# Kernel optimization log

Measured on AMD Instinct MI355X. Metric: run time of the kernel, lower is better.

Reference implementation:

```python
import jax, jax.numpy as jnp
import numpy as np

B, N, H = 8, 1024, 768
INNER = 64
ENT = 9
NEG = 1e12


def setup_inputs() -> dict:
    key = jax.random.key(0)
    ks = jax.random.split(key, 4)
    return {
        "last_hidden_state": jax.random.normal(ks[0], (B, N, H), dtype=jnp.float32),
        "attention_mask": jnp.ones((B, N), dtype=jnp.float32),
        "w1": jax.random.normal(ks[1], (H, 2 * INNER), dtype=jnp.float32) * 0.02,
        "b1": jnp.zeros((2 * INNER,), dtype=jnp.float32),
        "w2": jax.random.normal(ks[2], (H, 2 * ENT), dtype=jnp.float32) * 0.02,
        "b2": jnp.zeros((2 * ENT,), dtype=jnp.float32),
    }


def reference(last_hidden_state, attention_mask, w1, b1, w2, b2):
    b, n, _ = last_hidden_state.shape
    outputs = last_hidden_state @ w1 + b1            # (b, n, 2*inner)
    qw, kw = outputs[..., ::2], outputs[..., 1::2]   # (b, n, inner) each

    # Sinusoidal RoPE, 'zero' merge mode: even slots sin, odd slots cos
    half = INNER // 2
    inv_freq = jnp.power(10000.0, -2.0 * jnp.arange(half, dtype=jnp.float32) / INNER)
    ang = jnp.arange(n, dtype=jnp.float32)[:, None] * inv_freq[None, :]  # (n, half)
    sin_pos = jnp.repeat(jnp.sin(ang), 2, axis=-1)[None]  # (1, n, inner)
    cos_pos = jnp.repeat(jnp.cos(ang), 2, axis=-1)[None]

    def rope(x):
        # interleave (-x_odd, x_even)
        x2 = jnp.stack([-x[..., 1::2], x[..., ::2]], axis=-1).reshape(x.shape)
        return x * cos_pos + x2 * sin_pos

    qw, kw = rope(qw), rope(kw)

    logits = jnp.einsum('bmd,bnd->bmn', qw, kw) / jnp.sqrt(jnp.float32(INNER))
    bias = jnp.einsum('bnh->bhn', last_hidden_state @ w2 + b2) / 2.0  # (b, 2*ent, n)
    logits = logits[:, None] + bias[:, ::2, None] + bias[:, 1::2, :, None]  # (b,ent,n,n)

    # sequence masking on both trailing axes
    m = attention_mask.astype(logits.dtype)
    m_row = m[:, None, :, None]
    m_col = m[:, None, None, :]
    logits = logits * m_row + (-NEG) * (1.0 - m_row)
    logits = logits * m_col + (-NEG) * (1.0 - m_col)

    # strict lower-triangular suppression
    tril = jnp.tril(jnp.ones((n, n), dtype=logits.dtype), k=-1)
    logits = logits - tril * NEG
    return logits
```

## Files before the change

kernel.cpp:

```cpp
#include <hip/hip_runtime.h>
#include <cmath>

constexpr int kB = 8;
constexpr int kN = 1024;
constexpr int kH = 768;
constexpr float kNeg = 1000000000000.0f;

__global__ __launch_bounds__(256) void k1_proj_rope(
    const float* __restrict__ lhs, const float* __restrict__ w1,
    const float* __restrict__ b1, const float* __restrict__ w2,
    const float* __restrict__ b2, float* __restrict__ qw,
    float* __restrict__ kw, float* __restrict__ biasT)
{
  __shared__ float xs[16][kH];
  const int t = threadIdx.x;
  const int g0 = blockIdx.x * 16;

  const float4* lhs4 = reinterpret_cast<const float4*>(lhs + (size_t)g0 * kH);
  float4* xs4 = reinterpret_cast<float4*>(&xs[0][0]);
#pragma unroll
  for (int p = 0; p < 12; ++p) xs4[t + p * 256] = lhs4[t + p * 256];
  __syncthreads();

  const int c = t & 31;
  const int r2 = t >> 5;
  float acc0[4] = {0.f, 0.f, 0.f, 0.f};
  float acc1[4] = {0.f, 0.f, 0.f, 0.f};
  const float* xr0 = xs[r2];
  const float* xr1 = xs[r2 + 8];
  for (int h = 0; h < kH; h += 4) {
    float x0[4], x1[4];
    *reinterpret_cast<float4*>(x0) = *reinterpret_cast<const float4*>(&xr0[h]);
    *reinterpret_cast<float4*>(x1) = *reinterpret_cast<const float4*>(&xr1[h]);
#pragma unroll
    for (int hh = 0; hh < 4; ++hh) {
      const float4 wv =
          *reinterpret_cast<const float4*>(&w1[(size_t)(h + hh) * 128 + 4 * c]);
      acc0[0] += x0[hh] * wv.x; acc0[1] += x0[hh] * wv.y;
      acc0[2] += x0[hh] * wv.z; acc0[3] += x0[hh] * wv.w;
      acc1[0] += x1[hh] * wv.x; acc1[1] += x1[hh] * wv.y;
      acc1[2] += x1[hh] * wv.z; acc1[3] += x1[hh] * wv.w;
    }
  }
  float bb[4];
  *reinterpret_cast<float4*>(bb) = *reinterpret_cast<const float4*>(&b1[4 * c]);

  const float inv = exp2f(-(float)c * 0.41524101186092f);
#pragma unroll
  for (int rr = 0; rr < 2; ++rr) {
    const float* acc = rr ? acc1 : acc0;
    const int g = g0 + r2 + rr * 8;
    const int n = g & (kN - 1);
    float si, co;
    sincosf((float)n * inv, &si, &co);
    const float oq0 = acc[0] + bb[0], ok0 = acc[1] + bb[1];
    const float oq1 = acc[2] + bb[2], ok1 = acc[3] + bb[3];
    float2 qv = make_float2(oq0 * co - oq1 * si, oq1 * co + oq0 * si);
    float2 kv = make_float2(ok0 * co - ok1 * si, ok1 * co + ok0 * si);
    *reinterpret_cast<float2*>(&qw[(size_t)g * 64 + 2 * c]) = qv;
    *reinterpret_cast<float2*>(&kw[(size_t)g * 64 + 2 * c]) = kv;
  }

  for (int idx = t; idx < 288; idx += 256) {
    const int row = idx / 18, col = idx % 18;
    float s = 0.f;
    for (int h = 0; h < kH; h += 4) {
      const float4 xv = *reinterpret_cast<const float4*>(&xs[row][h]);
      s += xv.x * w2[(size_t)h * 18 + col];
      s += xv.y * w2[(size_t)(h + 1) * 18 + col];
      s += xv.z * w2[(size_t)(h + 2) * 18 + col];
      s += xv.w * w2[(size_t)(h + 3) * 18 + col];
    }
    const int g = g0 + row;
    const int b = g >> 10, n = g & (kN - 1);
    biasT[((size_t)b * 18 + col) * kN + n] = (s + b2[col]) * 0.5f;
  }
}

__global__ __launch_bounds__(256) void k2_logits(
    const float* __restrict__ qw, const float* __restrict__ kw,
    const float* __restrict__ biasT, const float* __restrict__ mask,
    float* __restrict__ out)
{
  constexpr int LD = 68;
  __shared__ float smem[64 * LD * 2 + 576 * 2 + 128];
  float* qs = smem;
  float* ks = smem + 64 * LD;
  float* ts = smem;
  float* bE = smem + 128 * LD;
  float* bO = bE + 576;
  float* mr_s = bO + 576;
  float* mc_s = mr_s + 64;

  const int t = threadIdx.x;
  const int b = blockIdx.z;
  const int m0 = blockIdx.y * 64;
  const int n0 = blockIdx.x * 64;

  const float* qg = qw + ((size_t)b * kN + m0) * 64;
  const float* kg = kw + ((size_t)b * kN + n0) * 64;
#pragma unroll
  for (int p = 0; p < 4; ++p) {
    const int idx = t + p * 256;
    const int row = idx >> 4;
    const int c4 = (idx & 15) << 2;
    *reinterpret_cast<float4*>(&qs[row * LD + c4]) =
        *reinterpret_cast<const float4*>(&qg[row * 64 + c4]);
    *reinterpret_cast<float4*>(&ks[row * LD + c4]) =
        *reinterpret_cast<const float4*>(&kg[row * 64 + c4]);
  }
  for (int idx = t; idx < 576; idx += 256) {
    const int e = idx >> 6, x = idx & 63;
    bE[idx] = biasT[((size_t)b * 18 + 2 * e) * kN + n0 + x];
    bO[idx] = biasT[((size_t)b * 18 + 2 * e + 1) * kN + m0 + x];
  }
  if (t < 64) mr_s[t] = mask[b * kN + m0 + t];
  else if (t < 128) mc_s[t - 64] = mask[b * kN + n0 + (t - 64)];
  __syncthreads();

  const int tx = t & 15;
  const int ty = t >> 4;
  const int ml = ty << 2;

  float acc[4][4] = {};
  for (int d = 0; d < 64; d += 4) {
    float4 q[4], k[4];
#pragma unroll
    for (int i = 0; i < 4; ++i)
      q[i] = *reinterpret_cast<const float4*>(&qs[(ml + i) * LD + d]);
#pragma unroll
    for (int j = 0; j < 4; ++j)
      k[j] = *reinterpret_cast<const float4*>(&ks[(tx + 16 * j) * LD + d]);
#pragma unroll
    for (int i = 0; i < 4; ++i)
#pragma unroll
      for (int j = 0; j < 4; ++j)
        acc[i][j] += q[i].x * k[j].x + q[i].y * k[j].y +
                     q[i].z * k[j].z + q[i].w * k[j].w;
  }

  __syncthreads();
#pragma unroll
  for (int i = 0; i < 4; ++i)
#pragma unroll
    for (int j = 0; j < 4; ++j)
      ts[(ml + i) * LD + tx + 16 * j] = acc[i][j] * 0.125f;
  __syncthreads();

  const int rb = ml;
  const int cb = tx << 2;
  float4 sv[4];
#pragma unroll
  for (int i = 0; i < 4; ++i)
    sv[i] = *reinterpret_cast<const float4*>(&ts[(rb + i) * LD + cb]);

  const float4 mrv = *reinterpret_cast<const float4*>(&mr_s[rb]);
  const float4 mcv = *reinterpret_cast<const float4*>(&mc_s[cb]);
  const float mrA[4] = {mrv.x, mrv.y, mrv.z, mrv.w};
  const float mcA[4] = {mcv.x, mcv.y, mcv.z, mcv.w};

  const size_t obase =
      (size_t)b * 9 * kN * kN + (size_t)(m0 + rb) * kN + (n0 + cb);
  for (int e = 0; e < 9; ++e) {
    const float4 bev = *reinterpret_cast<const float4*>(&bE[e * 64 + cb]);
    const float4 bov = *reinterpret_cast<const float4*>(&bO[e * 64 + rb]);
    const float beA[4] = {bev.x, bev.y, bev.z, bev.w};
    const float boA[4] = {bov.x, bov.y, bov.z, bov.w};
    float* oe = out + obase + (size_t)e * kN * kN;
#pragma unroll
    for (int i = 0; i < 4; ++i) {
      const int m = m0 + rb + i;
      const float* s = reinterpret_cast<const float*>(&sv[i]);
      float4 v4;
      float* v = reinterpret_cast<float*>(&v4);
#pragma unroll
      for (int c = 0; c < 4; ++c) {
        const int n = n0 + cb + c;
        float val = s[c] + beA[c] + boA[i];
        val = val * mrA[i] - kNeg * (1.f - mrA[i]);
        val = val * mcA[c] - kNeg * (1.f - mcA[c]);
        if (m > n) val -= kNeg;
        v[c] = val;
      }
      *reinterpret_cast<float4*>(&oe[(size_t)i * kN]) = v4;
    }
  }
}

extern "C" void kernel_launch(void* const* d_in, const int* in_sizes, int n_in,
                              void* d_out, int out_size, void* d_ws, size_t ws_size,
                              hipStream_t stream) {
  const float* lhs  = (const float*)d_in[0];
  const float* mask = (const float*)d_in[1];
  const float* w1   = (const float*)d_in[2];
  const float* b1   = (const float*)d_in[3];
  const float* w2   = (const float*)d_in[4];
  const float* b2   = (const float*)d_in[5];
  float* out = (float*)d_out;

  float* qw    = (float*)d_ws;
  float* kwp   = qw  + (size_t)kB * kN * 64;
  float* biasT = kwp + (size_t)kB * kN * 64;

  k1_proj_rope<<<dim3(kB * kN / 16), 256, 0, stream>>>(lhs, w1, b1, w2, b2,
                                                       qw, kwp, biasT);
  k2_logits<<<dim3(kN / 64, kN / 64, kB), 256, 0, stream>>>(qw, kwp, biasT,
                                                            mask, out);
}
```

Baseline: 428.9 us.

## Stage w1 chunks in shared memory and process 32 rows per projection block

The projection kernel now walks the hidden dimension in 96-wide chunks, staging each w1 chunk and the matching activation slice in shared memory, so w1 is read from LDS instead of global memory. Blocks grow to 512 threads covering 32 rows, and the w2 bias projection is spread over all threads chunk by chunk instead of being a serial tail done by a few threads. The output kernel only gets a loop variable renamed. The catch is an extra barrier per chunk and fewer blocks, while the dominant cost remains the large output write in the second kernel.

```diff
diff --git a/kernel.cpp b/kernel.cpp
--- a/kernel.cpp
+++ b/kernel.cpp
@@ -6,50 +6,93 @@
 constexpr int kH = 768;
 constexpr float kNeg = 1000000000000.0f;
 
-__global__ __launch_bounds__(256) void k1_proj_rope(
+__global__ __launch_bounds__(512) void k1_proj_rope(
     const float* __restrict__ lhs, const float* __restrict__ w1,
     const float* __restrict__ b1, const float* __restrict__ w2,
     const float* __restrict__ b2, float* __restrict__ qw,
     float* __restrict__ kw, float* __restrict__ biasT)
 {
-  __shared__ float xs[16][kH];
+  constexpr int CH = 96;
+  constexpr int XP = 100;
+  __shared__ float ws1[CH * 128];
+  __shared__ float xs[32 * XP];
+
   const int t = threadIdx.x;
-  const int g0 = blockIdx.x * 16;
-
-  const float4* lhs4 = reinterpret_cast<const float4*>(lhs + (size_t)g0 * kH);
-  float4* xs4 = reinterpret_cast<float4*>(&xs[0][0]);
-#pragma unroll
-  for (int p = 0; p < 12; ++p) xs4[t + p * 256] = lhs4[t + p * 256];
-  __syncthreads();
-
+  const int g0 = blockIdx.x * 32;
   const int c = t & 31;
-  const int r2 = t >> 5;
+  const int rp = t >> 5;
+
   float acc0[4] = {0.f, 0.f, 0.f, 0.f};
   float acc1[4] = {0.f, 0.f, 0.f, 0.f};
-  const float* xr0 = xs[r2];
-  const float* xr1 = xs[r2 + 8];
-  for (int h = 0; h < kH; h += 4) {
-    float x0[4], x1[4];
-    *reinterpret_cast<float4*>(x0) = *reinterpret_cast<const float4*>(&xr0[h]);
-    *reinterpret_cast<float4*>(x1) = *reinterpret_cast<const float4*>(&xr1[h]);
-#pragma unroll
-    for (int hh = 0; hh < 4; ++hh) {
-      const float4 wv =
-          *reinterpret_cast<const float4*>(&w1[(size_t)(h + hh) * 128 + 4 * c]);
-      acc0[0] += x0[hh] * wv.x; acc0[1] += x0[hh] * wv.y;
-      acc0[2] += x0[hh] * wv.z; acc0[3] += x0[hh] * wv.w;
-      acc1[0] += x1[hh] * wv.x; acc1[1] += x1[hh] * wv.y;
-      acc1[2] += x1[hh] * wv.z; acc1[3] += x1[hh] * wv.w;
-    }
-  }
+
+  const int row0 = t / 18, col0 = t % 18;
+  const int row1 = (t + 512) / 18, col1 = (t + 512) % 18;
+  float sb0 = 0.f, sb1 = 0.f;
+
+  for (int ch = 0; ch < 8; ++ch) {
+    const float4* w1g = reinterpret_cast<const float4*>(w1 + (size_t)ch * CH * 128);
+    float4* ws4 = reinterpret_cast<float4*>(ws1);
+#pragma unroll
+    for (int p = 0; p < 6; ++p) ws4[t + p * 512] = w1g[t + p * 512];
+#pragma unroll
+    for (int p = 0; p < 2; ++p) {
+      const int idx = t + p * 512;
+      if (idx < 768) {
+        const int row = idx / 24, c4 = idx % 24;
+        *reinterpret_cast<float4*>(&xs[row * XP + c4 * 4]) =
+            *reinterpret_cast<const float4*>(
+                &lhs[(size_t)(g0 + row) * kH + ch * CH + c4 * 4]);
+      }
+    }
+    __syncthreads();
+
+    const float* xr0 = &xs[rp * XP];
+    const float* xr1 = &xs[(rp + 16) * XP];
+    for (int h = 0; h < CH; h += 4) {
+      float x0[4], x1[4];
+      *reinterpret_cast<float4*>(x0) = *reinterpret_cast<const float4*>(&xr0[h]);
+      *reinterpret_cast<float4*>(x1) = *reinterpret_cast<const float4*>(&xr1[h]);
+#pragma unroll
+      for (int hh = 0; hh < 4; ++hh) {
+        const float4 wv = *reinterpret_cast<const float4*>(&ws1[(h + hh) * 128 + 4 * c]);
+        acc0[0] += x0[hh] * wv.x; acc0[1] += x0[hh] * wv.y;
+        acc0[2] += x0[hh] * wv.z; acc0[3] += x0[hh] * wv.w;
+        acc1[0] += x1[hh] * wv.x; acc1[1] += x1[hh] * wv.y;
+        acc1[2] += x1[hh] * wv.z; acc1[3] += x1[hh] * wv.w;
+      }
+    }
+
+    {
+      const int hb = ch * CH;
+      const float* xr = &xs[row0 * XP];
+      for (int h = 0; h < CH; h += 4) {
+        const float4 xv = *reinterpret_cast<const float4*>(&xr[h]);
+        sb0 += xv.x * w2[(size_t)(hb + h) * 18 + col0];
+        sb0 += xv.y * w2[(size_t)(hb + h + 1) * 18 + col0];
+        sb0 += xv.z * w2[(size_t)(hb + h + 2) * 18 + col0];
+        sb0 += xv.w * w2[(size_t)(hb + h + 3) * 18 + col0];
+      }
+      if (t < 64) {
+        const float* xr1b = &xs[row1 * XP];
+        for (int h = 0; h < CH; h += 4) {
+          const float4 xv = *reinterpret_cast<const float4*>(&xr1b[h]);
+          sb1 += xv.x * w2[(size_t)(hb + h) * 18 + col1];
+          sb1 += xv.y * w2[(size_t)(hb + h + 1) * 18 + col1];
+          sb1 += xv.z * w2[(size_t)(hb + h + 2) * 18 + col1];
+          sb1 += xv.w * w2[(size_t)(hb + h + 3) * 18 + col1];
+        }
+      }
+    }
+    __syncthreads();
+  }
+
   float bb[4];
   *reinterpret_cast<float4*>(bb) = *reinterpret_cast<const float4*>(&b1[4 * c]);
-
   const float inv = exp2f(-(float)c * 0.41524101186092f);
 #pragma unroll
   for (int rr = 0; rr < 2; ++rr) {
     const float* acc = rr ? acc1 : acc0;
-    const int g = g0 + r2 + rr * 8;
+    const int g = g0 + rp + rr * 16;
     const int n = g & (kN - 1);
     float si, co;
     sincosf((float)n * inv, &si, &co);
@@ -61,19 +104,15 @@
     *reinterpret_cast<float2*>(&kw[(size_t)g * 64 + 2 * c]) = kv;
   }
 
-  for (int idx = t; idx < 288; idx += 256) {
-    const int row = idx / 18, col = idx % 18;
-    float s = 0.f;
-    for (int h = 0; h < kH; h += 4) {
-      const float4 xv = *reinterpret_cast<const float4*>(&xs[row][h]);
-      s += xv.x * w2[(size_t)h * 18 + col];
-      s += xv.y * w2[(size_t)(h + 1) * 18 + col];
-      s += xv.z * w2[(size_t)(h + 2) * 18 + col];
-      s += xv.w * w2[(size_t)(h + 3) * 18 + col];
-    }
-    const int g = g0 + row;
+  {
+    const int g = g0 + row0;
     const int b = g >> 10, n = g & (kN - 1);
-    biasT[((size_t)b * 18 + col) * kN + n] = (s + b2[col]) * 0.5f;
+    biasT[((size_t)b * 18 + col0) * kN + n] = (sb0 + b2[col0]) * 0.5f;
+  }
+  if (t < 64) {
+    const int g = g0 + row1;
+    const int b = g >> 10, n = g & (kN - 1);
+    biasT[((size_t)b * 18 + col1) * kN + n] = (sb1 + b2[col1]) * 0.5f;
   }
 }
 
@@ -174,13 +213,13 @@
       float4 v4;
       float* v = reinterpret_cast<float*>(&v4);
 #pragma unroll
-      for (int c = 0; c < 4; ++c) {
-        const int n = n0 + cb + c;
-        float val = s[c] + beA[c] + boA[i];
+      for (int cc = 0; cc < 4; ++cc) {
+        const int n = n0 + cb + cc;
+        float val = s[cc] + beA[cc] + boA[i];
         val = val * mrA[i] - kNeg * (1.f - mrA[i]);
-        val = val * mcA[c] - kNeg * (1.f - mcA[c]);
+        val = val * mcA[cc] - kNeg * (1.f - mcA[cc]);
         if (m > n) val -= kNeg;
-        v[c] = val;
+        v[cc] = val;
       }
       *reinterpret_cast<float4*>(&oe[(size_t)i * kN]) = v4;
     }
@@ -202,7 +241,7 @@
   float* kwp   = qw  + (size_t)kB * kN * 64;
   float* biasT = kwp + (size_t)kB * kN * 64;
 
-  k1_proj_rope<<<dim3(kB * kN / 16), 256, 0, stream>>>(lhs, w1, b1, w2, b2,
+  k1_proj_rope<<<dim3(kB * kN / 32), 512, 0, stream>>>(lhs, w1, b1, w2, b2,
                                                        qw, kwp, biasT);
   k2_logits<<<dim3(kN / 64, kN / 64, kB), 256, 0, stream>>>(qw, kwp, biasT,
                                                             mask, out);
```

Result: no change. 426.8 us (-0.5%).
